# Kernel optimization log

Hardware: AMD Instinct MI355X
Metric: run time of the kernel (lower is better)

## Reference

```python
import jax, jax.numpy as jnp
import numpy as np

EPS = 1e-5

def setup_inputs() -> dict:
    key = jax.random.key(0)
    k0, k1 = jax.random.split(key, 2)
    N6, M5, M4 = 524288, 131072, 32768
    Cin, Cout = 256, 512
    data = jax.random.normal(k0, (N6, Cin), dtype=jnp.float32)
    weight = jax.random.normal(k1, (Cout, Cin), dtype=jnp.float32) * (1.0 / np.sqrt(Cin))
    gamma = jnp.ones((Cout,), dtype=jnp.float32)
    beta = jnp.zeros((Cout,), dtype=jnp.float32)
    # indices of non-empty nodes at the coarser depth (sorted, unique):
    # depth 6 has N6/8 = 65536 parents among M5 = 131072 depth-5 nodes (stride 2)
    idx5 = (jnp.arange(N6 // 8, dtype=jnp.int32) * (M5 // (N6 // 8)))
    # depth 5 has M5/8 = 16384 parents among M4 = 32768 depth-4 nodes (stride 2)
    idx4 = (jnp.arange(M5 // 8, dtype=jnp.int32) * (M4 // (M5 // 8)))
    return {"data": data, "weight": weight, "gamma": gamma, "beta": beta,
            "idx5": idx5, "idx4": idx4, "nnum5": M5, "nnum4": M4,
            "in_depth": 6, "out_depth": 4}

def _octree_max_pool(x, idx, nnum):
    # x: [N, C] child features in sibling groups of 8 -> pooled [N/8, C],
    # scattered (octree_pad) into the full coarser level of size nnum.
    N, C = x.shape
    y = x.reshape(N // 8, 8, C).max(axis=1)
    return jnp.zeros((nnum, C), x.dtype).at[idx].set(y)

def reference(data, weight, gamma, beta, idx5, idx4, nnum5, nnum4, in_depth, out_depth):
    out = data
    # in_depth (6) > out_depth (4): pool twice, then conv1x1+BN+ReLU
    for idx, nnum in ((idx5, nnum5), (idx4, nnum4)):
        out = _octree_max_pool(out, idx, nnum)
    h = out @ weight.T                      # 1x1 conv == bias-free linear
    mean = h.mean(axis=0)
    var = h.var(axis=0)
    h = (h - mean) * jax.lax.rsqrt(var + EPS) * gamma + beta
    return jax.nn.relu(h)
```

## Files before the change

### kernel.cpp

```cpp
#include <hip/hip_runtime.h>
#include <hip/hip_bf16.h>
#include <math.h>

#define CIN 256
#define COUT 512

typedef __attribute__((ext_vector_type(8))) short bf16x8;
typedef __attribute__((ext_vector_type(4))) float f32x4;
typedef __attribute__((ext_vector_type(4))) float f32x4v;

__device__ __forceinline__ ushort f2bf(float f) {
    union { float f; unsigned u; } x; x.f = f;
    unsigned r = x.u + 0x7FFFu + ((x.u >> 16) & 1u);
    return (ushort)(r >> 16);
}
__device__ __forceinline__ float bf2f(ushort u) {
    union { unsigned u; float f; } x; x.u = (unsigned)u << 16; return x.f;
}

__global__ __launch_bounds__(256) void prep_kernel(const int* __restrict__ idx5, int n_i5,
                                                   const int* __restrict__ idx4, int n_i4,
                                                   int n5, int n4,
                                                   int* __restrict__ inv5, int* __restrict__ inv4,
                                                   const float* __restrict__ W,
                                                   ushort* __restrict__ Wb, int wquads) {
    int t = blockIdx.x * blockDim.x + threadIdx.x;
    if (t < n_i5) {
        int s = idx5[t];
        inv5[s] = t;
        int e = (t + 1 < n_i5) ? idx5[t + 1] : n5;
        for (int k = s + 1; k < e; ++k) inv5[k] = -1;
        if (t == 0) for (int k = 0; k < s; ++k) inv5[k] = -1;
    } else if (t < n_i5 + n_i4) {
        int i = t - n_i5;
        int s = idx4[i];
        inv4[s] = i;
        int e = (i + 1 < n_i4) ? idx4[i + 1] : n4;
        for (int k = s + 1; k < e; ++k) inv4[k] = -1;
        if (i == 0) for (int k = 0; k < s; ++k) inv4[k] = -1;
    } else if (t < n_i5 + n_i4 + wquads) {
        int i = (t - n_i5 - n_i4) * 4;
        float4 v = *reinterpret_cast<const float4*>(W + i);
        ushort4 o;
        o.x = f2bf(v.x); o.y = f2bf(v.y); o.z = f2bf(v.z); o.w = f2bf(v.w);
        *reinterpret_cast<ushort4*>(&Wb[i]) = o;
    }
}

__global__ __launch_bounds__(256) void pool2_kernel(const float* __restrict__ data,
                                                    const int* __restrict__ inv5,
                                                    ushort* __restrict__ P, int G2) {
    int t = blockIdx.x * blockDim.x + threadIdx.x;
    int g = t >> 6;
    int q = t & 63;
    if (g >= G2) return;

    float4 acc = make_float4(-INFINITY, -INFINITY, -INFINITY, -INFINITY);
    bool any_empty = false;

    #pragma unroll
    for (int s = 0; s < 8; ++s) {
        int i = inv5[g * 8 + s];
        i = __builtin_amdgcn_readfirstlane(i);
        if (i >= 0) {
            const float* base = data + (size_t)i * 8 * CIN + q * 4;
            #pragma unroll
            for (int r = 0; r < 8; ++r) {
                f32x4v v = __builtin_nontemporal_load(
                    reinterpret_cast<const f32x4v*>(base + (size_t)r * CIN));
                acc.x = fmaxf(acc.x, v.x);
                acc.y = fmaxf(acc.y, v.y);
                acc.z = fmaxf(acc.z, v.z);
                acc.w = fmaxf(acc.w, v.w);
            }
        } else {
            any_empty = true;
        }
    }
    if (any_empty) {
        acc.x = fmaxf(acc.x, 0.f);
        acc.y = fmaxf(acc.y, 0.f);
        acc.z = fmaxf(acc.z, 0.f);
        acc.w = fmaxf(acc.w, 0.f);
    }
    ushort4 o;
    o.x = f2bf(acc.x); o.y = f2bf(acc.y); o.z = f2bf(acc.z); o.w = f2bf(acc.w);
    *reinterpret_cast<ushort4*>(&P[(size_t)g * CIN + q * 4]) = o;
}

__global__ __launch_bounds__(256) void mfma_gemm_kernel(const ushort* __restrict__ A,
                                                        const ushort* __restrict__ B,
                                                        ushort* __restrict__ H,
                                                        float* __restrict__ partial) {
    __shared__ __align__(16) ushort Asm[128 * 64];
    __shared__ __align__(16) ushort Bsm[128 * 64];

    int t = threadIdx.x;
    int lane = t & 63;
    int wid = t >> 6;
    int wm = wid >> 1, wn = wid & 1;
    int m0 = blockIdx.x * 128, n0 = blockIdx.y * 128;

    f32x4 acc[4][4] = {};

    for (int k0 = 0; k0 < CIN; k0 += 64) {
        #pragma unroll
        for (int i = 0; i < 4; ++i) {
            int idx = i * 256 + t;
            int row = idx >> 3;
            int sl  = idx & 7;
            bf16x8 av = *reinterpret_cast<const bf16x8*>(A + (size_t)(m0 + row) * CIN + k0 + sl * 8);
            bf16x8 bv = *reinterpret_cast<const bf16x8*>(B + (size_t)(n0 + row) * CIN + k0 + sl * 8);
            int ws = (sl ^ (row & 7)) * 8;
            *reinterpret_cast<bf16x8*>(&Asm[row * 64 + ws]) = av;
            *reinterpret_cast<bf16x8*>(&Bsm[row * 64 + ws]) = bv;
        }
        __syncthreads();

        #pragma unroll
        for (int ks = 0; ks < 2; ++ks) {
            bf16x8 af[4], bfr[4];
            int slog = ks * 4 + (lane >> 4);
            #pragma unroll
            for (int mi = 0; mi < 4; ++mi) {
                int row = wm * 64 + mi * 16 + (lane & 15);
                af[mi] = *reinterpret_cast<const bf16x8*>(&Asm[row * 64 + (slog ^ (row & 7)) * 8]);
            }
            #pragma unroll
            for (int ni = 0; ni < 4; ++ni) {
                int col = wn * 64 + ni * 16 + (lane & 15);
                bfr[ni] = *reinterpret_cast<const bf16x8*>(&Bsm[col * 64 + (slog ^ (col & 7)) * 8]);
            }
            #pragma unroll
            for (int mi = 0; mi < 4; ++mi)
                #pragma unroll
                for (int ni = 0; ni < 4; ++ni)
                    acc[mi][ni] = __builtin_amdgcn_mfma_f32_16x16x32_bf16(af[mi], bfr[ni], acc[mi][ni], 0, 0, 0);
        }
        __syncthreads();
    }

    float s[4], q[4];
    #pragma unroll
    for (int ni = 0; ni < 4; ++ni) {
        s[ni] = 0.f; q[ni] = 0.f;
        #pragma unroll
        for (int mi = 0; mi < 4; ++mi)
            #pragma unroll
            for (int r = 0; r < 4; ++r) {
                float v = acc[mi][ni][r];
                s[ni] += v;
                q[ni] = fmaf(v, v, q[ni]);
            }
        s[ni] += __shfl_xor(s[ni], 16);
        s[ni] += __shfl_xor(s[ni], 32);
        q[ni] += __shfl_xor(q[ni], 16);
        q[ni] += __shfl_xor(q[ni], 32);
    }
    float* redS = (float*)Asm;
    float* redQ = redS + 256;
    if (lane < 16) {
        #pragma unroll
        for (int ni = 0; ni < 4; ++ni) {
            int c = wn * 64 + ni * 16 + lane;
            redS[wm * 128 + c] = s[ni];
            redQ[wm * 128 + c] = q[ni];
        }
    }
    __syncthreads();
    if (t < 128) {
        float S = redS[t] + redS[128 + t];
        float Q = redQ[t] + redQ[128 + t];
        partial[(size_t)blockIdx.x * 1024 + blockIdx.y * 128 + t]       = S;
        partial[(size_t)blockIdx.x * 1024 + 512 + blockIdx.y * 128 + t] = Q;
    }

    #pragma unroll
    for (int mi = 0; mi < 4; ++mi) {
        #pragma unroll
        for (int ni = 0; ni < 4; ++ni) {
            int col   = n0 + wn * 64 + ni * 16 + (lane & 15);
            int rbase = m0 + wm * 64 + mi * 16 + (lane >> 4) * 4;
            #pragma unroll
            for (int r = 0; r < 4; ++r)
                H[(size_t)(rbase + r) * COUT + col] = f2bf(acc[mi][ni][r]);
        }
    }
}

__global__ __launch_bounds__(256) void bn_finalize_kernel(const float* __restrict__ partial, int nparts,
                                                          const float* __restrict__ gamma,
                                                          const float* __restrict__ beta,
                                                          float* __restrict__ scale,
                                                          float* __restrict__ shift,
                                                          float invN) {
    int c = blockIdx.x * blockDim.x + threadIdx.x;
    if (c >= COUT) return;
    float s = 0.f, q = 0.f;
    for (int p = 0; p < nparts; ++p) {
        s += partial[(size_t)p * 1024 + c];
        q += partial[(size_t)p * 1024 + 512 + c];
    }
    float mean = s * invN;
    float var  = fmaf(q, invN, -mean * mean);
    float inv  = rsqrtf(var + 1e-5f);
    float sc   = gamma[c] * inv;
    scale[c] = sc;
    shift[c] = fmaf(-mean, sc, beta[c]);
}

__global__ __launch_bounds__(256) void out_kernel(const ushort* __restrict__ H,
                                                  const int* __restrict__ inv4,
                                                  const float* __restrict__ scale,
                                                  const float* __restrict__ shift,
                                                  float* __restrict__ out, int rows) {
    int t = blockIdx.x * blockDim.x + threadIdx.x;
    int m = t >> 7;
    int qd = t & 127;
    if (m >= rows) return;
    int c = qd * 4;
    int j = inv4[m];
    float4 sc = *reinterpret_cast<const float4*>(&scale[c]);
    float4 sh = *reinterpret_cast<const float4*>(&shift[c]);
    float4 r;
    if (j >= 0) {
        ushort4 h = *reinterpret_cast<const ushort4*>(&H[(size_t)j * COUT + c]);
        r.x = fmaxf(fmaf(bf2f(h.x), sc.x, sh.x), 0.f);
        r.y = fmaxf(fmaf(bf2f(h.y), sc.y, sh.y), 0.f);
        r.z = fmaxf(fmaf(bf2f(h.z), sc.z, sh.z), 0.f);
        r.w = fmaxf(fmaf(bf2f(h.w), sc.w, sh.w), 0.f);
    } else {
        r.x = fmaxf(sh.x, 0.f);
        r.y = fmaxf(sh.y, 0.f);
        r.z = fmaxf(sh.z, 0.f);
        r.w = fmaxf(sh.w, 0.f);
    }
    *reinterpret_cast<float4*>(&out[(size_t)m * COUT + c]) = r;
}

extern "C" void kernel_launch(void* const* d_in, const int* in_sizes, int n_in,
                              void* d_out, int out_size, void* d_ws, size_t ws_size,
                              hipStream_t stream) {
    const float* data   = (const float*)d_in[0];
    const float* weight = (const float*)d_in[1];
    const float* gamma  = (const float*)d_in[2];
    const float* beta   = (const float*)d_in[3];
    const int*   idx5   = (const int*)d_in[4];
    const int*   idx4   = (const int*)d_in[5];

    const int n_i5 = in_sizes[4];
    const int n_i4 = in_sizes[5];
    const int G2   = n_i4;
    const int n5   = 8 * n_i4;
    const int rows = out_size / COUT;
    const int M    = G2;
    const int MB   = M / 128;

    char* w = (char*)d_ws;
    ushort* P      = (ushort*)w;                        w += (size_t)G2 * CIN * sizeof(ushort);
    ushort* H      = (ushort*)w;                        w += (size_t)G2 * COUT * sizeof(ushort);
    ushort* Wb     = (ushort*)w;                        w += (size_t)COUT * CIN * sizeof(ushort);
    float* partial = (float*)w;                         w += (size_t)MB * 1024 * sizeof(float);
    float* scale   = (float*)w;                         w += COUT * sizeof(float);
    float* shift   = (float*)w;                         w += COUT * sizeof(float);
    int*   inv5    = (int*)w;                           w += (size_t)n5 * sizeof(int);
    int*   inv4    = (int*)w;                           w += (size_t)rows * sizeof(int);

    const int wquads = COUT * CIN / 4;

    {
        int n = n_i5 + n_i4 + wquads;
        prep_kernel<<<(n + 255) / 256, 256, 0, stream>>>(idx5, n_i5, idx4, n_i4, n5, rows,
                                                         inv5, inv4, weight, Wb, wquads);
    }
    pool2_kernel<<<(G2 * 64 + 255) / 256, 256, 0, stream>>>(data, inv5, P, G2);
    {
        dim3 grid(MB, COUT / 128);
        mfma_gemm_kernel<<<grid, 256, 0, stream>>>(P, Wb, H, partial);
    }
    bn_finalize_kernel<<<2, 256, 0, stream>>>(partial, MB, gamma, beta, scale, shift,
                                              1.0f / (float)rows);
    out_kernel<<<((size_t)rows * 128 + 255) / 256, 256, 0, stream>>>(H, inv4, scale, shift,
                                                                     (float*)d_out, rows);
}
```

Measured before the change: 155.9 us.

## Fuse pooling, GEMM, BN and output into one cooperative mega-kernel

Replaces five kernel launches with a single cooperative kernel. Each block pools 64 rows into LDS, converts W to bf16 in registers, runs MFMA, writes BN partials, and uses grid syncs to finalize the statistics before applying BN+ReLU from registers. This removes the P and H round-trips through global memory and the launch gaps. In exchange it needs all 256 blocks co-resident for the grid sync, and every block reconverts the full weight slice from fp32.

Result: slower. 276.2 us (+77.2%).

```diff
diff --git a/kernel.cpp b/kernel.cpp
--- a/kernel.cpp
+++ b/kernel.cpp
@@ -1,6 +1,9 @@
 #include <hip/hip_runtime.h>
 #include <hip/hip_bf16.h>
+#include <hip/hip_cooperative_groups.h>
 #include <math.h>
+
+namespace cg = cooperative_groups;
 
 #define CIN 256
 #define COUT 512
@@ -14,228 +17,212 @@
     unsigned r = x.u + 0x7FFFu + ((x.u >> 16) & 1u);
     return (ushort)(r >> 16);
 }
-__device__ __forceinline__ float bf2f(ushort u) {
-    union { unsigned u; float f; } x; x.u = (unsigned)u << 16; return x.f;
-}
-
-__global__ __launch_bounds__(256) void prep_kernel(const int* __restrict__ idx5, int n_i5,
-                                                   const int* __restrict__ idx4, int n_i4,
-                                                   int n5, int n4,
-                                                   int* __restrict__ inv5, int* __restrict__ inv4,
-                                                   const float* __restrict__ W,
-                                                   ushort* __restrict__ Wb, int wquads) {
-    int t = blockIdx.x * blockDim.x + threadIdx.x;
-    if (t < n_i5) {
-        int s = idx5[t];
-        inv5[s] = t;
-        int e = (t + 1 < n_i5) ? idx5[t + 1] : n5;
-        for (int k = s + 1; k < e; ++k) inv5[k] = -1;
-        if (t == 0) for (int k = 0; k < s; ++k) inv5[k] = -1;
-    } else if (t < n_i5 + n_i4) {
-        int i = t - n_i5;
-        int s = idx4[i];
-        inv4[s] = i;
-        int e = (i + 1 < n_i4) ? idx4[i + 1] : n4;
-        for (int k = s + 1; k < e; ++k) inv4[k] = -1;
-        if (i == 0) for (int k = 0; k < s; ++k) inv4[k] = -1;
-    } else if (t < n_i5 + n_i4 + wquads) {
-        int i = (t - n_i5 - n_i4) * 4;
-        float4 v = *reinterpret_cast<const float4*>(W + i);
+
+__device__ __forceinline__ int bsearch_eq(const int* __restrict__ arr, int n, int key) {
+    int lo = 0, hi = n - 1;
+    while (lo <= hi) {
+        int mid = (lo + hi) >> 1;
+        int v = arr[mid];
+        if (v == key) return mid;
+        if (v < key) lo = mid + 1; else hi = mid - 1;
+    }
+    return -1;
+}
+
+__global__ __launch_bounds__(512, 2) void mega_kernel(
+    const float* __restrict__ data,
+    const float* __restrict__ W,
+    const float* __restrict__ gamma,
+    const float* __restrict__ beta,
+    const int*   __restrict__ idx5, int n_i5,
+    const int*   __restrict__ idx4, int n_i4,
+    float* __restrict__ partial,
+    float* __restrict__ scaleg,
+    float* __restrict__ shiftg,
+    float* __restrict__ out,
+    float invN, int rows_out)
+{
+    __shared__ __align__(16) union {
+        ushort A[64 * 256];
+        float  outb[16][516];
+    } u;
+    __shared__ int   inv5_l[512];
+    __shared__ int   inv4_l[128];
+    __shared__ float scl[512], sht[512], rsht[512];
+    __shared__ float wred[16];
+
+    const int b    = blockIdx.x;
+    const int t    = threadIdx.x;
+    const int lane = t & 63;
+    const int w    = t >> 6;
+    const int g0   = b * 64;
+    const int orpb = rows_out / gridDim.x;
+
+    if (t < 512) inv5_l[t] = bsearch_eq(idx5, n_i5, g0 * 8 + t);
+    if (t < 128) inv4_l[t] = bsearch_eq(idx4, n_i4, b * orpb + t);
+    __syncthreads();
+
+    for (int j = 0; j < 8; ++j) {
+        int row = w * 8 + j;
+        float4 acc = make_float4(-INFINITY, -INFINITY, -INFINITY, -INFINITY);
+        bool any_empty = false;
+        #pragma unroll
+        for (int s = 0; s < 8; ++s) {
+            int i = inv5_l[row * 8 + s];
+            i = __builtin_amdgcn_readfirstlane(i);
+            if (i >= 0) {
+                const float* base = data + (size_t)i * (8 * CIN) + lane * 4;
+                #pragma unroll
+                for (int r = 0; r < 8; ++r) {
+                    f32x4v v = __builtin_nontemporal_load(
+                        reinterpret_cast<const f32x4v*>(base + (size_t)r * CIN));
+                    acc.x = fmaxf(acc.x, v.x);
+                    acc.y = fmaxf(acc.y, v.y);
+                    acc.z = fmaxf(acc.z, v.z);
+                    acc.w = fmaxf(acc.w, v.w);
+                }
+            } else {
+                any_empty = true;
+            }
+        }
+        if (any_empty) {
+            acc.x = fmaxf(acc.x, 0.f);
+            acc.y = fmaxf(acc.y, 0.f);
+            acc.z = fmaxf(acc.z, 0.f);
+            acc.w = fmaxf(acc.w, 0.f);
+        }
         ushort4 o;
-        o.x = f2bf(v.x); o.y = f2bf(v.y); o.z = f2bf(v.z); o.w = f2bf(v.w);
-        *reinterpret_cast<ushort4*>(&Wb[i]) = o;
-    }
-}
-
-__global__ __launch_bounds__(256) void pool2_kernel(const float* __restrict__ data,
-                                                    const int* __restrict__ inv5,
-                                                    ushort* __restrict__ P, int G2) {
-    int t = blockIdx.x * blockDim.x + threadIdx.x;
-    int g = t >> 6;
-    int q = t & 63;
-    if (g >= G2) return;
-
-    float4 acc = make_float4(-INFINITY, -INFINITY, -INFINITY, -INFINITY);
-    bool any_empty = false;
-
-    #pragma unroll
-    for (int s = 0; s < 8; ++s) {
-        int i = inv5[g * 8 + s];
-        i = __builtin_amdgcn_readfirstlane(i);
-        if (i >= 0) {
-            const float* base = data + (size_t)i * 8 * CIN + q * 4;
-            #pragma unroll
-            for (int r = 0; r < 8; ++r) {
-                f32x4v v = __builtin_nontemporal_load(
-                    reinterpret_cast<const f32x4v*>(base + (size_t)r * CIN));
-                acc.x = fmaxf(acc.x, v.x);
-                acc.y = fmaxf(acc.y, v.y);
-                acc.z = fmaxf(acc.z, v.z);
-                acc.w = fmaxf(acc.w, v.w);
-            }
-        } else {
-            any_empty = true;
-        }
-    }
-    if (any_empty) {
-        acc.x = fmaxf(acc.x, 0.f);
-        acc.y = fmaxf(acc.y, 0.f);
-        acc.z = fmaxf(acc.z, 0.f);
-        acc.w = fmaxf(acc.w, 0.f);
-    }
-    ushort4 o;
-    o.x = f2bf(acc.x); o.y = f2bf(acc.y); o.z = f2bf(acc.z); o.w = f2bf(acc.w);
-    *reinterpret_cast<ushort4*>(&P[(size_t)g * CIN + q * 4]) = o;
-}
-
-__global__ __launch_bounds__(256) void mfma_gemm_kernel(const ushort* __restrict__ A,
-                                                        const ushort* __restrict__ B,
-                                                        ushort* __restrict__ H,
-                                                        float* __restrict__ partial) {
-    __shared__ __align__(16) ushort Asm[128 * 64];
-    __shared__ __align__(16) ushort Bsm[128 * 64];
-
-    int t = threadIdx.x;
-    int lane = t & 63;
-    int wid = t >> 6;
-    int wm = wid >> 1, wn = wid & 1;
-    int m0 = blockIdx.x * 128, n0 = blockIdx.y * 128;
-
-    f32x4 acc[4][4] = {};
-
-    for (int k0 = 0; k0 < CIN; k0 += 64) {
-        #pragma unroll
-        for (int i = 0; i < 4; ++i) {
-            int idx = i * 256 + t;
-            int row = idx >> 3;
-            int sl  = idx & 7;
-            bf16x8 av = *reinterpret_cast<const bf16x8*>(A + (size_t)(m0 + row) * CIN + k0 + sl * 8);
-            bf16x8 bv = *reinterpret_cast<const bf16x8*>(B + (size_t)(n0 + row) * CIN + k0 + sl * 8);
-            int ws = (sl ^ (row & 7)) * 8;
-            *reinterpret_cast<bf16x8*>(&Asm[row * 64 + ws]) = av;
-            *reinterpret_cast<bf16x8*>(&Bsm[row * 64 + ws]) = bv;
-        }
-        __syncthreads();
-
-        #pragma unroll
-        for (int ks = 0; ks < 2; ++ks) {
-            bf16x8 af[4], bfr[4];
-            int slog = ks * 4 + (lane >> 4);
-            #pragma unroll
-            for (int mi = 0; mi < 4; ++mi) {
-                int row = wm * 64 + mi * 16 + (lane & 15);
-                af[mi] = *reinterpret_cast<const bf16x8*>(&Asm[row * 64 + (slog ^ (row & 7)) * 8]);
-            }
-            #pragma unroll
-            for (int ni = 0; ni < 4; ++ni) {
-                int col = wn * 64 + ni * 16 + (lane & 15);
-                bfr[ni] = *reinterpret_cast<const bf16x8*>(&Bsm[col * 64 + (slog ^ (col & 7)) * 8]);
-            }
-            #pragma unroll
-            for (int mi = 0; mi < 4; ++mi)
-                #pragma unroll
-                for (int ni = 0; ni < 4; ++ni)
-                    acc[mi][ni] = __builtin_amdgcn_mfma_f32_16x16x32_bf16(af[mi], bfr[ni], acc[mi][ni], 0, 0, 0);
-        }
-        __syncthreads();
-    }
-
-    float s[4], q[4];
+        o.x = f2bf(acc.x); o.y = f2bf(acc.y); o.z = f2bf(acc.z); o.w = f2bf(acc.w);
+        int g16 = lane >> 1, h = lane & 1;
+        int us  = row * 256 + ((g16 ^ (row & 7)) << 3) + h * 4;
+        *reinterpret_cast<ushort4*>(&u.A[us]) = o;
+    }
+
+    bf16x8 bfr[4][8];
     #pragma unroll
     for (int ni = 0; ni < 4; ++ni) {
-        s[ni] = 0.f; q[ni] = 0.f;
+        int col = w * 64 + ni * 16 + (lane & 15);
+        const float* wrow = W + (size_t)col * CIN + (lane >> 4) * 8;
+        #pragma unroll
+        for (int ks = 0; ks < 8; ++ks) {
+            float4 lo = *reinterpret_cast<const float4*>(wrow + ks * 32);
+            float4 hi = *reinterpret_cast<const float4*>(wrow + ks * 32 + 4);
+            bf16x8 f;
+            f[0] = (short)f2bf(lo.x); f[1] = (short)f2bf(lo.y);
+            f[2] = (short)f2bf(lo.z); f[3] = (short)f2bf(lo.w);
+            f[4] = (short)f2bf(hi.x); f[5] = (short)f2bf(hi.y);
+            f[6] = (short)f2bf(hi.z); f[7] = (short)f2bf(hi.w);
+            bfr[ni][ks] = f;
+        }
+    }
+    __syncthreads();
+
+    f32x4 acc[4][4] = {};
+    #pragma unroll
+    for (int ks = 0; ks < 8; ++ks) {
+        bf16x8 af[4];
+        #pragma unroll
+        for (int mi = 0; mi < 4; ++mi) {
+            int row = mi * 16 + (lane & 15);
+            int sl  = ks * 4 + (lane >> 4);
+            af[mi] = *reinterpret_cast<const bf16x8*>(&u.A[row * 256 + ((sl ^ (row & 7)) << 3)]);
+        }
+        #pragma unroll
+        for (int mi = 0; mi < 4; ++mi)
+            #pragma unroll
+            for (int ni = 0; ni < 4; ++ni)
+                acc[mi][ni] = __builtin_amdgcn_mfma_f32_16x16x32_bf16(af[mi], bfr[ni][ks], acc[mi][ni], 0, 0, 0);
+    }
+
+    #pragma unroll
+    for (int ni = 0; ni < 4; ++ni) {
+        float s = 0.f, q = 0.f;
         #pragma unroll
         for (int mi = 0; mi < 4; ++mi)
             #pragma unroll
             for (int r = 0; r < 4; ++r) {
                 float v = acc[mi][ni][r];
-                s[ni] += v;
-                q[ni] = fmaf(v, v, q[ni]);
+                s += v;
+                q = fmaf(v, v, q);
             }
-        s[ni] += __shfl_xor(s[ni], 16);
-        s[ni] += __shfl_xor(s[ni], 32);
-        q[ni] += __shfl_xor(q[ni], 16);
-        q[ni] += __shfl_xor(q[ni], 32);
-    }
-    float* redS = (float*)Asm;
-    float* redQ = redS + 256;
-    if (lane < 16) {
+        s += __shfl_xor(s, 16); s += __shfl_xor(s, 32);
+        q += __shfl_xor(q, 16); q += __shfl_xor(q, 32);
+        if (lane < 16) {
+            int c = w * 64 + ni * 16 + lane;
+            partial[(size_t)b * 1024 + c]       = s;
+            partial[(size_t)b * 1024 + 512 + c] = q;
+        }
+    }
+    __threadfence();
+    cg::this_grid().sync();
+
+    {
+        int c = 2 * b + (t >> 8);
+        int p = t & 255;
+        float S = partial[(size_t)p * 1024 + c];
+        float Q = partial[(size_t)p * 1024 + 512 + c];
+        #pragma unroll
+        for (int off = 1; off < 64; off <<= 1) {
+            S += __shfl_xor(S, off);
+            Q += __shfl_xor(Q, off);
+        }
+        if (lane == 0) { wred[w * 2] = S; wred[w * 2 + 1] = Q; }
+        __syncthreads();
+        if (t == 0 || t == 256) {
+            int cc   = 2 * b + (t >> 8);
+            int base = (t >> 8) * 8;
+            float S = wred[base + 0] + wred[base + 2] + wred[base + 4] + wred[base + 6];
+            float Q = wred[base + 1] + wred[base + 3] + wred[base + 5] + wred[base + 7];
+            float mean = S * invN;
+            float var  = fmaf(Q, invN, -mean * mean);
+            float inv  = rsqrtf(var + 1e-5f);
+            float sc   = gamma[cc] * inv;
+            scaleg[cc] = sc;
+            shiftg[cc] = fmaf(-mean, sc, beta[cc]);
+        }
+    }
+    __threadfence();
+    cg::this_grid().sync();
+
+    if (t < 512) {
+        float s = scaleg[t], h = shiftg[t];
+        scl[t] = s; sht[t] = h; rsht[t] = fmaxf(h, 0.f);
+    }
+    __syncthreads();
+
+    for (int mi = 0; mi < 4; ++mi) {
         #pragma unroll
         for (int ni = 0; ni < 4; ++ni) {
-            int c = wn * 64 + ni * 16 + lane;
-            redS[wm * 128 + c] = s[ni];
-            redQ[wm * 128 + c] = q[ni];
-        }
-    }
-    __syncthreads();
-    if (t < 128) {
-        float S = redS[t] + redS[128 + t];
-        float Q = redQ[t] + redQ[128 + t];
-        partial[(size_t)blockIdx.x * 1024 + blockIdx.y * 128 + t]       = S;
-        partial[(size_t)blockIdx.x * 1024 + 512 + blockIdx.y * 128 + t] = Q;
-    }
-
-    #pragma unroll
-    for (int mi = 0; mi < 4; ++mi) {
-        #pragma unroll
-        for (int ni = 0; ni < 4; ++ni) {
-            int col   = n0 + wn * 64 + ni * 16 + (lane & 15);
-            int rbase = m0 + wm * 64 + mi * 16 + (lane >> 4) * 4;
+            int col = w * 64 + ni * 16 + (lane & 15);
+            float s = scl[col], h = sht[col];
+            int r0 = (lane >> 4) * 4;
             #pragma unroll
             for (int r = 0; r < 4; ++r)
-                H[(size_t)(rbase + r) * COUT + col] = f2bf(acc[mi][ni][r]);
-        }
-    }
-}
-
-__global__ __launch_bounds__(256) void bn_finalize_kernel(const float* __restrict__ partial, int nparts,
-                                                          const float* __restrict__ gamma,
-                                                          const float* __restrict__ beta,
-                                                          float* __restrict__ scale,
-                                                          float* __restrict__ shift,
-                                                          float invN) {
-    int c = blockIdx.x * blockDim.x + threadIdx.x;
-    if (c >= COUT) return;
-    float s = 0.f, q = 0.f;
-    for (int p = 0; p < nparts; ++p) {
-        s += partial[(size_t)p * 1024 + c];
-        q += partial[(size_t)p * 1024 + 512 + c];
-    }
-    float mean = s * invN;
-    float var  = fmaf(q, invN, -mean * mean);
-    float inv  = rsqrtf(var + 1e-5f);
-    float sc   = gamma[c] * inv;
-    scale[c] = sc;
-    shift[c] = fmaf(-mean, sc, beta[c]);
-}
-
-__global__ __launch_bounds__(256) void out_kernel(const ushort* __restrict__ H,
-                                                  const int* __restrict__ inv4,
-                                                  const float* __restrict__ scale,
-                                                  const float* __restrict__ shift,
-                                                  float* __restrict__ out, int rows) {
-    int t = blockIdx.x * blockDim.x + threadIdx.x;
-    int m = t >> 7;
-    int qd = t & 127;
-    if (m >= rows) return;
-    int c = qd * 4;
-    int j = inv4[m];
-    float4 sc = *reinterpret_cast<const float4*>(&scale[c]);
-    float4 sh = *reinterpret_cast<const float4*>(&shift[c]);
-    float4 r;
-    if (j >= 0) {
-        ushort4 h = *reinterpret_cast<const ushort4*>(&H[(size_t)j * COUT + c]);
-        r.x = fmaxf(fmaf(bf2f(h.x), sc.x, sh.x), 0.f);
-        r.y = fmaxf(fmaf(bf2f(h.y), sc.y, sh.y), 0.f);
-        r.z = fmaxf(fmaf(bf2f(h.z), sc.z, sh.z), 0.f);
-        r.w = fmaxf(fmaf(bf2f(h.w), sc.w, sh.w), 0.f);
-    } else {
-        r.x = fmaxf(sh.x, 0.f);
-        r.y = fmaxf(sh.y, 0.f);
-        r.z = fmaxf(sh.z, 0.f);
-        r.w = fmaxf(sh.w, 0.f);
-    }
-    *reinterpret_cast<float4*>(&out[(size_t)m * COUT + c]) = r;
+                u.outb[r0 + r][col] = fmaxf(fmaf(acc[mi][ni][r], s, h), 0.f);
+        }
+        __syncthreads();
+        {
+            int row = t >> 5;
+            int j   = t & 31;
+            int gr  = idx4[g0 + mi * 16 + row];
+            float* orow = out + (size_t)gr * COUT;
+            #pragma unroll
+            for (int i = 0; i < 4; ++i) {
+                int c = j * 4 + i * 128;
+                *reinterpret_cast<float4*>(orow + c) = *reinterpret_cast<float4*>(&u.outb[row][c]);
+            }
+        }
+        __syncthreads();
+    }
+
+    for (int base = 0; base < orpb; base += 4) {
+        int rl = base + (t >> 7);
+        if (inv4_l[rl] < 0) {
+            int c = (t & 127) * 4;
+            *reinterpret_cast<float4*>(out + (size_t)(b * orpb + rl) * COUT + c) =
+                *reinterpret_cast<float4*>(&rsht[c]);
+        }
+    }
 }
 
 extern "C" void kernel_launch(void* const* d_in, const int* in_sizes, int n_in,
@@ -248,38 +235,23 @@
     const int*   idx5   = (const int*)d_in[4];
     const int*   idx4   = (const int*)d_in[5];
 
-    const int n_i5 = in_sizes[4];
-    const int n_i4 = in_sizes[5];
-    const int G2   = n_i4;
-    const int n5   = 8 * n_i4;
-    const int rows = out_size / COUT;
-    const int M    = G2;
-    const int MB   = M / 128;
-
-    char* w = (char*)d_ws;
-    ushort* P      = (ushort*)w;                        w += (size_t)G2 * CIN * sizeof(ushort);
-    ushort* H      = (ushort*)w;                        w += (size_t)G2 * COUT * sizeof(ushort);
-    ushort* Wb     = (ushort*)w;                        w += (size_t)COUT * CIN * sizeof(ushort);
-    float* partial = (float*)w;                         w += (size_t)MB * 1024 * sizeof(float);
-    float* scale   = (float*)w;                         w += COUT * sizeof(float);
-    float* shift   = (float*)w;                         w += COUT * sizeof(float);
-    int*   inv5    = (int*)w;                           w += (size_t)n5 * sizeof(int);
-    int*   inv4    = (int*)w;                           w += (size_t)rows * sizeof(int);
-
-    const int wquads = COUT * CIN / 4;
-
-    {
-        int n = n_i5 + n_i4 + wquads;
-        prep_kernel<<<(n + 255) / 256, 256, 0, stream>>>(idx5, n_i5, idx4, n_i4, n5, rows,
-                                                         inv5, inv4, weight, Wb, wquads);
-    }
-    pool2_kernel<<<(G2 * 64 + 255) / 256, 256, 0, stream>>>(data, inv5, P, G2);
-    {
-        dim3 grid(MB, COUT / 128);
-        mfma_gemm_kernel<<<grid, 256, 0, stream>>>(P, Wb, H, partial);
-    }
-    bn_finalize_kernel<<<2, 256, 0, stream>>>(partial, MB, gamma, beta, scale, shift,
-                                              1.0f / (float)rows);
-    out_kernel<<<((size_t)rows * 128 + 255) / 256, 256, 0, stream>>>(H, inv4, scale, shift,
-                                                                     (float*)d_out, rows);
-}
+    int n_i5 = in_sizes[4];
+    int n_i4 = in_sizes[5];
+    int rows = out_size / COUT;
+    int nblocks = n_i4 / 64;
+
+    float* partial = (float*)d_ws;
+    float* scaleg  = partial + (size_t)nblocks * 1024;
+    float* shiftg  = scaleg + COUT;
+    float* outp    = (float*)d_out;
+    float  invN    = 1.0f / (float)rows;
+
+    void* args[] = {
+        (void*)&data, (void*)&weight, (void*)&gamma, (void*)&beta,
+        (void*)&idx5, (void*)&n_i5, (void*)&idx4, (void*)&n_i4,
+        (void*)&partial, (void*)&scaleg, (void*)&shiftg,
+        (void*)&outp, (void*)&invN, (void*)&rows
+    };
+    hipLaunchCooperativeKernel((void*)mega_kernel, dim3(nblocks), dim3(512),
+                               args, 0, stream);
+}
```
